# Optimization experiments

Measured on AMD Instinct MI355X. Metric: run time of the kernel, lower is better.

The kernel has to match this reference:

```python
import jax, jax.numpy as jnp
import numpy as np

EPS = 1e-5  # torch LayerNorm default

def _ln(x, g, b):
    m = jnp.mean(x, axis=-1, keepdims=True)
    v = jnp.var(x, axis=-1, keepdims=True)
    return (x - m) / jnp.sqrt(v + EPS) * g + b

def setup_inputs() -> dict:
    B, S, F, H = 32, 512, 32, 128
    key = jax.random.key(0)
    ks = jax.random.split(key, 20)
    sc = 0.05
    inp = {
        "x": jax.random.normal(ks[0], (B, S, F), dtype=jnp.float32),
        # per-feature GRNs, stacked along F. fc1: Linear(1,H) -> weight vec (F,H)
        "fw1": jax.random.normal(ks[1], (F, H), dtype=jnp.float32) * sc,
        "fb1": jax.random.normal(ks[2], (F, H), dtype=jnp.float32) * sc,
        "fw2": jax.random.normal(ks[3], (F, H, H), dtype=jnp.float32) * sc,
        "fb2": jax.random.normal(ks[4], (F, H), dtype=jnp.float32) * sc,
        "fglu_w": jax.random.normal(ks[5], (F, H, 2 * H), dtype=jnp.float32) * sc,
        "fglu_b": jax.random.normal(ks[6], (F, 2 * H), dtype=jnp.float32) * sc,
        "fskip": jax.random.normal(ks[7], (F, H), dtype=jnp.float32) * sc,  # skip_proj Linear(1,H,bias=False)
        "fln_g": jnp.ones((F, H), dtype=jnp.float32),
        "fln_b": jnp.zeros((F, H), dtype=jnp.float32),
        # weight GRN: Linear(F,H)->ELU->Linear(H,F)->GLU(F)->LN(F); skip is identity (F==F)
        "ww1": jax.random.normal(ks[8], (F, H), dtype=jnp.float32) * sc,
        "wb1": jax.random.normal(ks[9], (H,), dtype=jnp.float32) * sc,
        "ww2": jax.random.normal(ks[10], (H, F), dtype=jnp.float32) * sc,
        "wb2": jax.random.normal(ks[11], (F,), dtype=jnp.float32) * sc,
        "wglu_w": jax.random.normal(ks[12], (F, 2 * F), dtype=jnp.float32) * sc,
        "wglu_b": jax.random.normal(ks[13], (2 * F,), dtype=jnp.float32) * sc,
        "wln_g": jnp.ones((F,), dtype=jnp.float32),
        "wln_b": jnp.zeros((F,), dtype=jnp.float32),
    }
    return inp

def reference(x, fw1, fb1, fw2, fb2, fglu_w, fglu_b, fskip, fln_g, fln_b,
              ww1, wb1, ww2, wb2, wglu_w, wglu_b, wln_g, wln_b):
    # ---- per-feature GRNs, batched over the F axis (dropout = eval, identity) ----
    # fc1(Linear(1,H)) + ELU : x[...,f] is a scalar per token
    h = jax.nn.elu(x[..., None] * fw1 + fb1)                 # (B,S,F,H)
    h = jnp.einsum('bsfh,fho->bsfo', h, fw2) + fb2           # fc2 (B,S,F,H)
    g = jnp.einsum('bsfh,fho->bsfo', h, fglu_w) + fglu_b     # GLU pre-act (B,S,F,2H)
    v, gate = jnp.split(g, 2, axis=-1)
    glu = v * jax.nn.sigmoid(gate)                           # (B,S,F,H)
    skip = x[..., None] * fskip                              # skip_proj (B,S,F,H)
    processed = _ln(glu + skip, fln_g[None, None], fln_b[None, None])  # (B,S,F,H)

    # ---- weight GRN over the full feature vector ----
    wh = jax.nn.elu(jnp.einsum('bsf,fh->bsh', x, ww1) + wb1)  # (B,S,H)
    wh = jnp.einsum('bsh,hf->bsf', wh, ww2) + wb2             # (B,S,F)
    wg = jnp.einsum('bsf,fg->bsg', wh, wglu_w) + wglu_b       # (B,S,2F)
    wv, wgate = jnp.split(wg, 2, axis=-1)
    wglu = wv * jax.nn.sigmoid(wgate)
    w = _ln(wglu + x, wln_g, wln_b)                           # skip is identity (F==F)
    weights = jax.nn.softmax(w, axis=-1)                      # (B,S,F)

    out = jnp.einsum('bsf,bsfh->bsh', weights, processed)     # weighted combine
    return (out, weights)
```

## Files before the change

kernel.cpp:

```cpp
#include <hip/hip_runtime.h>
#include <cstdint>
#include <cstddef>

#define NTOK 16384
#define FDIM 32
#define HDIM 128
#define TOKB 32

typedef __attribute__((ext_vector_type(8))) short short8;
typedef __attribute__((ext_vector_type(4))) float float4v;
typedef __attribute__((ext_vector_type(2))) float float2v;
typedef __attribute__((ext_vector_type(4))) unsigned int uint4v;

__device__ __forceinline__ float elu_f(float x)  { return x > 0.f ? x : __expf(x) - 1.f; }
__device__ __forceinline__ float sigm_f(float x) { return 1.f / (1.f + __expf(-x)); }

__device__ __forceinline__ unsigned int f2bf(float f) {
  unsigned int u = __float_as_uint(f);
  u += 0x7FFFu + ((u >> 16) & 1u);
  return u >> 16;
}
__device__ __forceinline__ unsigned int cvtpk(float lo, float hi) {
  unsigned int r;
  asm("v_cvt_pk_bf16_f32 %0, %1, %2" : "=v"(r) : "v"(lo), "v"(hi));
  return r;
}

__global__ __launch_bounds__(256) void k_pw(
    const float* __restrict__ x,
    const float* __restrict__ fw2, const float* __restrict__ fb2,
    const float* __restrict__ fglu_w, const float* __restrict__ fglu_b,
    const float* __restrict__ fskip, const float* __restrict__ flng,
    const float* __restrict__ flnb,
    const float* __restrict__ ww1, const float* __restrict__ wb1,
    const float* __restrict__ ww2, const float* __restrict__ wb2,
    const float* __restrict__ wglu_w, const float* __restrict__ wglu_b,
    const float* __restrict__ wln_g, const float* __restrict__ wln_b,
    unsigned short* __restrict__ bfrag, float* __restrict__ scal,
    float* __restrict__ wout)
{
  __shared__ __align__(16) float smem[4096];
  const int tid = threadIdx.x;

  if (blockIdx.x < 128) {
    const int f  = blockIdx.x >> 2;
    const int ks = blockIdx.x & 3;
    const float* src = fw2 + ((size_t)f * 128 + ks * 32) * 128;
    for (int i = 0; i < 4; ++i) {
      int vi = tid + i * 256;
      *(float4v*)&smem[vi * 4] = *(const float4v*)&src[vi * 4];
    }
    __syncthreads();

    const int o2 = tid;
    float acc[32];
#pragma unroll
    for (int kk = 0; kk < 32; ++kk) acc[kk] = 0.f;
    float bacc = 0.f;

    for (int o = 0; o < 128; o += 4) {
      float gv0 = fglu_w[((size_t)f * 128 + o + 0) * 256 + o2];
      float gv1 = fglu_w[((size_t)f * 128 + o + 1) * 256 + o2];
      float gv2 = fglu_w[((size_t)f * 128 + o + 2) * 256 + o2];
      float gv3 = fglu_w[((size_t)f * 128 + o + 3) * 256 + o2];
      bacc += fb2[f * 128 + o + 0] * gv0 + fb2[f * 128 + o + 1] * gv1
            + fb2[f * 128 + o + 2] * gv2 + fb2[f * 128 + o + 3] * gv3;
#pragma unroll
      for (int kk = 0; kk < 32; ++kk) {
        float4v a4 = *(const float4v*)&smem[kk * 128 + o];
        acc[kk] += a4[0] * gv0 + a4[1] * gv1 + a4[2] * gv2 + a4[3] * gv3;
      }
    }

    const int type = o2 >> 7;
    const int h    = o2 & 127;
    const int w2   = h >> 4;
    const int r    = h & 15;
    const size_t tbase = ((((size_t)f * 8 + w2) * 2 + type) * 4 + ks) * 512;
#pragma unroll
    for (int gg = 0; gg < 4; ++gg) {
      uint4v pk;
      pk[0] = f2bf(acc[gg * 8 + 0]) | (f2bf(acc[gg * 8 + 1]) << 16);
      pk[1] = f2bf(acc[gg * 8 + 2]) | (f2bf(acc[gg * 8 + 3]) << 16);
      pk[2] = f2bf(acc[gg * 8 + 4]) | (f2bf(acc[gg * 8 + 5]) << 16);
      pk[3] = f2bf(acc[gg * 8 + 6]) | (f2bf(acc[gg * 8 + 7]) << 16);
      *(uint4v*)(bfrag + tbase + (size_t)(r + gg * 16) * 8) = pk;
    }
    if (ks == 0) {
      scal[f * 640 + type * 128 + h] = bacc + fglu_b[f * 256 + o2];
      if (type == 0) {
        scal[f * 640 + 256 + h] = fskip[f * 128 + h];
        scal[f * 640 + 384 + h] = flng[f * 128 + h];
        scal[f * 640 + 512 + h] = flnb[f * 128 + h];
      }
    }

  } else {
    const int bid = blockIdx.x - 128;
    const int wv  = tid >> 6;
    const int l   = tid & 63;
    const int t   = bid * 4 + wv;
    float* S = smem + wv * 256;

    float xv = x[(size_t)t * 32 + (l & 31)];
    if (l < 32) S[l] = xv;
    float a0 = wb1[l], a1 = wb1[l + 64];
    __syncthreads();
    for (int f2 = 0; f2 < 32; ++f2) {
      float xf = S[f2];
      a0 = fmaf(xf, ww1[f2 * 128 + l], a0);
      a1 = fmaf(xf, ww1[f2 * 128 + l + 64], a1);
    }
    a0 = elu_f(a0); a1 = elu_f(a1);
    S[32 + l] = a0; S[32 + l + 64] = a1;
    __syncthreads();

    const int o    = l & 31;
    const int half = l >> 5;
    float b = 0.f;
    for (int hh = 0; hh < 64; ++hh)
      b = fmaf(S[32 + half * 64 + hh], ww2[(half * 64 + hh) * 32 + o], b);
    b += __shfl_xor(b, 32);
    b += wb2[o];
    S[160 + o] = b;
    __syncthreads();

    float g = wglu_b[l];
    for (int o2i = 0; o2i < 32; ++o2i)
      g = fmaf(S[160 + o2i], wglu_w[o2i * 64 + l], g);

    float gate = __shfl_xor(g, 32);
    float y = g * sigm_f(gate) + xv;
    float s = y;
    s += __shfl_xor(s, 1); s += __shfl_xor(s, 2); s += __shfl_xor(s, 4);
    s += __shfl_xor(s, 8); s += __shfl_xor(s, 16);
    float mean = s * (1.f / 32.f);
    float d = y - mean;
    float ss = d * d;
    ss += __shfl_xor(ss, 1); ss += __shfl_xor(ss, 2); ss += __shfl_xor(ss, 4);
    ss += __shfl_xor(ss, 8); ss += __shfl_xor(ss, 16);
    float rstd = rsqrtf(ss * (1.f / 32.f) + 1e-5f);
    const int cc = l & 31;
    float ln = d * rstd * wln_g[cc] + wln_b[cc];
    float mx = ln;
    mx = fmaxf(mx, __shfl_xor(mx, 1));  mx = fmaxf(mx, __shfl_xor(mx, 2));
    mx = fmaxf(mx, __shfl_xor(mx, 4));  mx = fmaxf(mx, __shfl_xor(mx, 8));
    mx = fmaxf(mx, __shfl_xor(mx, 16));
    float e = __expf(ln - mx);
    float se = e;
    se += __shfl_xor(se, 1); se += __shfl_xor(se, 2); se += __shfl_xor(se, 4);
    se += __shfl_xor(se, 8); se += __shfl_xor(se, 16);
    if (l < 32) wout[(size_t)t * 32 + l] = e / se;
  }
}

__global__ __launch_bounds__(512, 4) void k_main(
    const float* __restrict__ x,
    const float* __restrict__ fw1, const float* __restrict__ fb1,
    const unsigned short* __restrict__ bfrag, const float* __restrict__ scal,
    const float* __restrict__ wts, float* __restrict__ out)
{
  __shared__ __align__(16) unsigned short a_lds[2][TOKB * 128];
  __shared__ __align__(16) float x_lds[FDIM * TOKB];
  __shared__ __align__(16) float w_lds[FDIM * TOKB];
  __shared__ __align__(16) float sred[3][2][TOKB];

  const int tid = threadIdx.x;
  const int w   = tid >> 6;
  const int l   = tid & 63;
  const int tk  = l & 15;
  const int rg  = l >> 4;
  const int t0  = blockIdx.x * TOKB;
  const int h0  = w * 16 + rg * 4;
  const int st  = tid >> 4;
  const int sk  = (tid & 15) * 8;
  const int stg_byte = (st * 256 + sk * 2) ^ ((st & 7) << 4);

  {
    float2v xv = *(const float2v*)(x   + (size_t)t0 * FDIM + tid * 2);
    float2v wv = *(const float2v*)(wts + (size_t)t0 * FDIM + tid * 2);
#pragma unroll
    for (int e = 0; e < 2; ++e) {
      int flat = tid * 2 + e;
      int tt = flat >> 5, ff = flat & 31;
      x_lds[ff * TOKB + tt] = xv[e];
      w_lds[ff * TOKB + tt] = wv[e];
    }
    if (tid < 192) ((float*)sred)[tid] = 0.f;
  }

  float4v oa0 = (float4v){0.f, 0.f, 0.f, 0.f};
  float4v oa1 = (float4v){0.f, 0.f, 0.f, 0.f};
  float4v py0, py1, plg, plb;
  float pwt0 = 0.f, pwt1 = 0.f;

  __syncthreads();

  int cb = 0;
#pragma unroll 1
  for (int f = 0; f < FDIM; ++f) {
    short8 aV[4], aG[4];
    {
      const unsigned short* bb = bfrag + (((size_t)f * 8 + w) * 8) * 512 + (size_t)l * 8;
#pragma unroll
      for (int ks = 0; ks < 4; ++ks) {
        aV[ks] = *(const short8*)(bb + (size_t)ks * 512);
        aG[ks] = *(const short8*)(bb + (size_t)(4 + ks) * 512);
      }
    }
    const float* sp = scal + (size_t)f * 640 + h0;
    float4v bcv = *(const float4v*)(sp);
    float4v bcg = *(const float4v*)(sp + 128);
    float4v fs4 = *(const float4v*)(sp + 256);
    float4v lg4 = *(const float4v*)(sp + 384);
    float4v lb4 = *(const float4v*)(sp + 512);
    float xt0 = x_lds[f * TOKB + tk],      wt0 = w_lds[f * TOKB + tk];
    float xt1 = x_lds[f * TOKB + 16 + tk], wt1 = w_lds[f * TOKB + 16 + tk];

    {
      float xf = x_lds[f * TOKB + st];
      float4v w1a = *(const float4v*)(fw1 + f * HDIM + sk);
      float4v w1b = *(const float4v*)(fw1 + f * HDIM + sk + 4);
      float4v b1a = *(const float4v*)(fb1 + f * HDIM + sk);
      float4v b1b = *(const float4v*)(fb1 + f * HDIM + sk + 4);
      uint4v pk;
      pk[0] = cvtpk(elu_f(fmaf(xf, w1a[0], b1a[0])),
                    elu_f(fmaf(xf, w1a[1], b1a[1])));
      pk[1] = cvtpk(elu_f(fmaf(xf, w1a[2], b1a[2])),
                    elu_f(fmaf(xf, w1a[3], b1a[3])));
      pk[2] = cvtpk(elu_f(fmaf(xf, w1b[0], b1b[0])),
                    elu_f(fmaf(xf, w1b[1], b1b[1])));
      pk[3] = cvtpk(elu_f(fmaf(xf, w1b[2], b1b[2])),
                    elu_f(fmaf(xf, w1b[3], b1b[3])));
      *(uint4v*)((char*)a_lds[f & 1] + stg_byte) = pk;
    }

    __syncthreads();

    float4v av0 = (float4v){0.f,0.f,0.f,0.f}, ag0 = av0, av1 = av0, ag1 = av0;
#pragma unroll
    for (int ks = 0; ks < 4; ++ks) {
      int b0 = tk * 256 + (ks * 32 + rg * 8) * 2;
      b0 ^= (tk & 7) << 4;
      short8 hf0 = *(const short8*)((const char*)a_lds[f & 1] + b0);
      int b1 = (16 + tk) * 256 + (ks * 32 + rg * 8) * 2;
      b1 ^= (tk & 7) << 4;
      short8 hf1 = *(const short8*)((const char*)a_lds[f & 1] + b1);
      av0 = __builtin_amdgcn_mfma_f32_16x16x32_bf16(aV[ks], hf0, av0, 0, 0, 0);
      ag0 = __builtin_amdgcn_mfma_f32_16x16x32_bf16(aG[ks], hf0, ag0, 0, 0, 0);
      av1 = __builtin_amdgcn_mfma_f32_16x16x32_bf16(aV[ks], hf1, av1, 0, 0, 0);
      ag1 = __builtin_amdgcn_mfma_f32_16x16x32_bf16(aG[ks], hf1, ag1, 0, 0, 0);
    }

    if (f > 0) {
      const int pb = (cb == 0) ? 2 : cb - 1;
      float sA  = sred[pb][0][tk],      ssA = sred[pb][1][tk];
      float sB  = sred[pb][0][16 + tk], ssB = sred[pb][1][16 + tk];
      float m0 = sA * (1.f / 128.f);
      float m1 = sB * (1.f / 128.f);
      float v0 = fmaf(-m0, m0, ssA * (1.f / 128.f));
      float v1 = fmaf(-m1, m1, ssB * (1.f / 128.f));
      float rw0 = rsqrtf(v0 + 1e-5f) * pwt0;
      float rw1 = rsqrtf(v1 + 1e-5f) * pwt1;
#pragma unroll
      for (int i = 0; i < 4; ++i) {
        oa0[i] = fmaf((py0[i] - m0) * rw0, plg[i], fmaf(pwt0, plb[i], oa0[i]));
        oa1[i] = fmaf((py1[i] - m1) * rw1, plg[i], fmaf(pwt1, plb[i], oa1[i]));
      }
    }

    float s0 = 0.f, ss0 = 0.f, s1 = 0.f, ss1 = 0.f;
#pragma unroll
    for (int i = 0; i < 4; ++i) {
      float ya = fmaf(xt0, fs4[i], (av0[i] + bcv[i]) * sigm_f(ag0[i] + bcg[i]));
      float yb = fmaf(xt1, fs4[i], (av1[i] + bcv[i]) * sigm_f(ag1[i] + bcg[i]));
      py0[i] = ya; py1[i] = yb;
      s0 += ya; ss0 = fmaf(ya, ya, ss0);
      s1 += yb; ss1 = fmaf(yb, yb, ss1);
    }
    s0  += __shfl_xor(s0, 16);  s0  += __shfl_xor(s0, 32);
    ss0 += __shfl_xor(ss0, 16); ss0 += __shfl_xor(ss0, 32);
    s1  += __shfl_xor(s1, 16);  s1  += __shfl_xor(s1, 32);
    ss1 += __shfl_xor(ss1, 16); ss1 += __shfl_xor(ss1, 32);
    if (rg == 0) {
      atomicAdd(&sred[cb][0][tk], s0);
      atomicAdd(&sred[cb][0][16 + tk], s1);
    } else if (rg == 1) {
      atomicAdd(&sred[cb][1][tk], ss0);
      atomicAdd(&sred[cb][1][16 + tk], ss1);
    }
    {
      const int nb = (cb == 2) ? 0 : cb + 1;
      if (tid < 64) ((float*)(sred[nb]))[tid] = 0.f;
    }

    pwt0 = wt0; pwt1 = wt1; plg = lg4; plb = lb4;
    cb = (cb == 2) ? 0 : cb + 1;
  }

  __syncthreads();
  {
    const int pb = (cb == 0) ? 2 : cb - 1;
    float sA  = sred[pb][0][tk],      ssA = sred[pb][1][tk];
    float sB  = sred[pb][0][16 + tk], ssB = sred[pb][1][16 + tk];
    float m0 = sA * (1.f / 128.f);
    float m1 = sB * (1.f / 128.f);
    float v0 = fmaf(-m0, m0, ssA * (1.f / 128.f));
    float v1 = fmaf(-m1, m1, ssB * (1.f / 128.f));
    float rw0 = rsqrtf(v0 + 1e-5f) * pwt0;
    float rw1 = rsqrtf(v1 + 1e-5f) * pwt1;
#pragma unroll
    for (int i = 0; i < 4; ++i) {
      oa0[i] = fmaf((py0[i] - m0) * rw0, plg[i], fmaf(pwt0, plb[i], oa0[i]));
      oa1[i] = fmaf((py1[i] - m1) * rw1, plg[i], fmaf(pwt1, plb[i], oa1[i]));
    }
  }

  *(float4v*)(out + (size_t)(t0 + tk) * HDIM + h0)      = oa0;
  *(float4v*)(out + (size_t)(t0 + 16 + tk) * HDIM + h0) = oa1;
}

extern "C" void kernel_launch(void* const* d_in, const int* in_sizes, int n_in,
                              void* d_out, int out_size, void* d_ws, size_t ws_size,
                              hipStream_t stream) {
  const float* x      = (const float*)d_in[0];
  const float* fw1    = (const float*)d_in[1];
  const float* fb1    = (const float*)d_in[2];
  const float* fw2    = (const float*)d_in[3];
  const float* fb2    = (const float*)d_in[4];
  const float* fglu_w = (const float*)d_in[5];
  const float* fglu_b = (const float*)d_in[6];
  const float* fskip  = (const float*)d_in[7];
  const float* fln_g  = (const float*)d_in[8];
  const float* fln_b  = (const float*)d_in[9];
  const float* ww1    = (const float*)d_in[10];
  const float* wb1    = (const float*)d_in[11];
  const float* ww2    = (const float*)d_in[12];
  const float* wb2    = (const float*)d_in[13];
  const float* wglu_w = (const float*)d_in[14];
  const float* wglu_b = (const float*)d_in[15];
  const float* wln_g  = (const float*)d_in[16];
  const float* wln_b  = (const float*)d_in[17];

  float* outp = (float*)d_out;
  float* wout = outp + (size_t)NTOK * HDIM;

  unsigned short* bfrag = (unsigned short*)d_ws;
  float* scal = (float*)((char*)d_ws + (size_t)2 * 1024 * 1024);

  k_pw<<<dim3(128 + NTOK / 4), dim3(256), 0, stream>>>(
      x, fw2, fb2, fglu_w, fglu_b, fskip, fln_g, fln_b,
      ww1, wb1, ww2, wb2, wglu_w, wglu_b, wln_g, wln_b,
      bfrag, scal, wout);
  k_main<<<dim3(NTOK / TOKB), dim3(512), 0, stream>>>(
      x, fw1, fb1, bfrag, scal, wout, outp);
}
```

Baseline: 143.7 us.

## Process two features per loop iteration to halve block barriers

The main loop now handles two features per iteration. Both feature tiles are staged into four LDS buffers, with one __syncthreads per pair instead of one per feature. The LayerNorm reduction buffers and deferred-combine state are duplicated so each pair's statistics are applied one iteration later. This cuts barrier count and lengthens the independent work between barriers, at the cost of more registers and LDS, which may hurt occupancy under launch_bounds(512,4).

```diff
diff --git a/kernel.cpp b/kernel.cpp
--- a/kernel.cpp
+++ b/kernel.cpp
@@ -160,10 +160,10 @@
     const unsigned short* __restrict__ bfrag, const float* __restrict__ scal,
     const float* __restrict__ wts, float* __restrict__ out)
 {
-  __shared__ __align__(16) unsigned short a_lds[2][TOKB * 128];
+  __shared__ __align__(16) unsigned short a_lds[4][TOKB * 128];
   __shared__ __align__(16) float x_lds[FDIM * TOKB];
   __shared__ __align__(16) float w_lds[FDIM * TOKB];
-  __shared__ __align__(16) float sred[3][2][TOKB];
+  __shared__ __align__(16) float sred[3][2][2][TOKB];
 
   const int tid = threadIdx.x;
   const int w   = tid >> 6;
@@ -186,43 +186,39 @@
       x_lds[ff * TOKB + tt] = xv[e];
       w_lds[ff * TOKB + tt] = wv[e];
     }
-    if (tid < 192) ((float*)sred)[tid] = 0.f;
+    if (tid < 384) ((float*)sred)[tid] = 0.f;
   }
 
   float4v oa0 = (float4v){0.f, 0.f, 0.f, 0.f};
   float4v oa1 = (float4v){0.f, 0.f, 0.f, 0.f};
-  float4v py0, py1, plg, plb;
-  float pwt0 = 0.f, pwt1 = 0.f;
+  float4v pyA0 = oa0, pyA1 = oa0, pyB0 = oa0, pyB1 = oa0;
+  float4v plgA = oa0, plbA = oa0, plgB = oa0, plbB = oa0;
+  float pwtA0 = 0.f, pwtA1 = 0.f, pwtB0 = 0.f, pwtB1 = 0.f;
 
   __syncthreads();
 
-  int cb = 0;
+  int p = 0;
 #pragma unroll 1
-  for (int f = 0; f < FDIM; ++f) {
+  for (int k = 0; k < FDIM / 2; ++k) {
+    const int g    = 2 * k;
+    const int bufp = (k & 1) * 2;
+
     short8 aV[4], aG[4];
     {
-      const unsigned short* bb = bfrag + (((size_t)f * 8 + w) * 8) * 512 + (size_t)l * 8;
+      const unsigned short* bb = bfrag + (((size_t)g * 8 + w) * 8) * 512 + (size_t)l * 8;
 #pragma unroll
       for (int ks = 0; ks < 4; ++ks) {
         aV[ks] = *(const short8*)(bb + (size_t)ks * 512);
         aG[ks] = *(const short8*)(bb + (size_t)(4 + ks) * 512);
       }
     }
-    const float* sp = scal + (size_t)f * 640 + h0;
-    float4v bcv = *(const float4v*)(sp);
-    float4v bcg = *(const float4v*)(sp + 128);
-    float4v fs4 = *(const float4v*)(sp + 256);
-    float4v lg4 = *(const float4v*)(sp + 384);
-    float4v lb4 = *(const float4v*)(sp + 512);
-    float xt0 = x_lds[f * TOKB + tk],      wt0 = w_lds[f * TOKB + tk];
-    float xt1 = x_lds[f * TOKB + 16 + tk], wt1 = w_lds[f * TOKB + 16 + tk];
-
-    {
-      float xf = x_lds[f * TOKB + st];
-      float4v w1a = *(const float4v*)(fw1 + f * HDIM + sk);
-      float4v w1b = *(const float4v*)(fw1 + f * HDIM + sk + 4);
-      float4v b1a = *(const float4v*)(fb1 + f * HDIM + sk);
-      float4v b1b = *(const float4v*)(fb1 + f * HDIM + sk + 4);
+
+    {
+      float xf = x_lds[g * TOKB + st];
+      float4v w1a = *(const float4v*)(fw1 + g * HDIM + sk);
+      float4v w1b = *(const float4v*)(fw1 + g * HDIM + sk + 4);
+      float4v b1a = *(const float4v*)(fb1 + g * HDIM + sk);
+      float4v b1b = *(const float4v*)(fb1 + g * HDIM + sk + 4);
       uint4v pk;
       pk[0] = cvtpk(elu_f(fmaf(xf, w1a[0], b1a[0])),
                     elu_f(fmaf(xf, w1a[1], b1a[1])));
@@ -232,87 +228,206 @@
                     elu_f(fmaf(xf, w1b[1], b1b[1])));
       pk[3] = cvtpk(elu_f(fmaf(xf, w1b[2], b1b[2])),
                     elu_f(fmaf(xf, w1b[3], b1b[3])));
-      *(uint4v*)((char*)a_lds[f & 1] + stg_byte) = pk;
+      *(uint4v*)((char*)a_lds[bufp] + stg_byte) = pk;
+    }
+    {
+      float xf = x_lds[(g + 1) * TOKB + st];
+      float4v w1a = *(const float4v*)(fw1 + (g + 1) * HDIM + sk);
+      float4v w1b = *(const float4v*)(fw1 + (g + 1) * HDIM + sk + 4);
+      float4v b1a = *(const float4v*)(fb1 + (g + 1) * HDIM + sk);
+      float4v b1b = *(const float4v*)(fb1 + (g + 1) * HDIM + sk + 4);
+      uint4v pk;
+      pk[0] = cvtpk(elu_f(fmaf(xf, w1a[0], b1a[0])),
+                    elu_f(fmaf(xf, w1a[1], b1a[1])));
+      pk[1] = cvtpk(elu_f(fmaf(xf, w1a[2], b1a[2])),
+                    elu_f(fmaf(xf, w1a[3], b1a[3])));
+      pk[2] = cvtpk(elu_f(fmaf(xf, w1b[0], b1b[0])),
+                    elu_f(fmaf(xf, w1b[1], b1b[1])));
+      pk[3] = cvtpk(elu_f(fmaf(xf, w1b[2], b1b[2])),
+                    elu_f(fmaf(xf, w1b[3], b1b[3])));
+      *(uint4v*)((char*)a_lds[bufp + 1] + stg_byte) = pk;
     }
 
     __syncthreads();
 
-    float4v av0 = (float4v){0.f,0.f,0.f,0.f}, ag0 = av0, av1 = av0, ag1 = av0;
-#pragma unroll
-    for (int ks = 0; ks < 4; ++ks) {
-      int b0 = tk * 256 + (ks * 32 + rg * 8) * 2;
-      b0 ^= (tk & 7) << 4;
-      short8 hf0 = *(const short8*)((const char*)a_lds[f & 1] + b0);
-      int b1 = (16 + tk) * 256 + (ks * 32 + rg * 8) * 2;
-      b1 ^= (tk & 7) << 4;
-      short8 hf1 = *(const short8*)((const char*)a_lds[f & 1] + b1);
-      av0 = __builtin_amdgcn_mfma_f32_16x16x32_bf16(aV[ks], hf0, av0, 0, 0, 0);
-      ag0 = __builtin_amdgcn_mfma_f32_16x16x32_bf16(aG[ks], hf0, ag0, 0, 0, 0);
-      av1 = __builtin_amdgcn_mfma_f32_16x16x32_bf16(aV[ks], hf1, av1, 0, 0, 0);
-      ag1 = __builtin_amdgcn_mfma_f32_16x16x32_bf16(aG[ks], hf1, ag1, 0, 0, 0);
-    }
-
-    if (f > 0) {
-      const int pb = (cb == 0) ? 2 : cb - 1;
-      float sA  = sred[pb][0][tk],      ssA = sred[pb][1][tk];
-      float sB  = sred[pb][0][16 + tk], ssB = sred[pb][1][16 + tk];
+    if (k > 0) {
+      const int pp = (p == 0) ? 2 : p - 1;
+      {
+        float sA  = sred[pp][0][0][tk],      ssA = sred[pp][0][1][tk];
+        float sB  = sred[pp][0][0][16 + tk], ssB = sred[pp][0][1][16 + tk];
+        float m0 = sA * (1.f / 128.f);
+        float m1 = sB * (1.f / 128.f);
+        float v0 = fmaf(-m0, m0, ssA * (1.f / 128.f));
+        float v1 = fmaf(-m1, m1, ssB * (1.f / 128.f));
+        float rw0 = rsqrtf(v0 + 1e-5f) * pwtA0;
+        float rw1 = rsqrtf(v1 + 1e-5f) * pwtA1;
+#pragma unroll
+        for (int i = 0; i < 4; ++i) {
+          oa0[i] = fmaf((pyA0[i] - m0) * rw0, plgA[i], fmaf(pwtA0, plbA[i], oa0[i]));
+          oa1[i] = fmaf((pyA1[i] - m1) * rw1, plgA[i], fmaf(pwtA1, plbA[i], oa1[i]));
+        }
+      }
+      {
+        float sA  = sred[pp][1][0][tk],      ssA = sred[pp][1][1][tk];
+        float sB  = sred[pp][1][0][16 + tk], ssB = sred[pp][1][1][16 + tk];
+        float m0 = sA * (1.f / 128.f);
+        float m1 = sB * (1.f / 128.f);
+        float v0 = fmaf(-m0, m0, ssA * (1.f / 128.f));
+        float v1 = fmaf(-m1, m1, ssB * (1.f / 128.f));
+        float rw0 = rsqrtf(v0 + 1e-5f) * pwtB0;
+        float rw1 = rsqrtf(v1 + 1e-5f) * pwtB1;
+#pragma unroll
+        for (int i = 0; i < 4; ++i) {
+          oa0[i] = fmaf((pyB0[i] - m0) * rw0, plgB[i], fmaf(pwtB0, plbB[i], oa0[i]));
+          oa1[i] = fmaf((pyB1[i] - m1) * rw1, plgB[i], fmaf(pwtB1, plbB[i], oa1[i]));
+        }
+      }
+    }
+
+    {
+      const float* sp = scal + (size_t)g * 640 + h0;
+      float4v bcv = *(const float4v*)(sp);
+      float4v bcg = *(const float4v*)(sp + 128);
+      float4v fs4 = *(const float4v*)(sp + 256);
+      float4v lg4 = *(const float4v*)(sp + 384);
+      float4v lb4 = *(const float4v*)(sp + 512);
+
+      float4v av0 = (float4v){0.f,0.f,0.f,0.f}, ag0 = av0, av1 = av0, ag1 = av0;
+#pragma unroll
+      for (int ks = 0; ks < 4; ++ks) {
+        int b0 = tk * 256 + (ks * 32 + rg * 8) * 2;
+        b0 ^= (tk & 7) << 4;
+        short8 hf0 = *(const short8*)((const char*)a_lds[bufp] + b0);
+        int b1 = (16 + tk) * 256 + (ks * 32 + rg * 8) * 2;
+        b1 ^= (tk & 7) << 4;
+        short8 hf1 = *(const short8*)((const char*)a_lds[bufp] + b1);
+        av0 = __builtin_amdgcn_mfma_f32_16x16x32_bf16(aV[ks], hf0, av0, 0, 0, 0);
+        ag0 = __builtin_amdgcn_mfma_f32_16x16x32_bf16(aG[ks], hf0, ag0, 0, 0, 0);
+        av1 = __builtin_amdgcn_mfma_f32_16x16x32_bf16(aV[ks], hf1, av1, 0, 0, 0);
+        ag1 = __builtin_amdgcn_mfma_f32_16x16x32_bf16(aG[ks], hf1, ag1, 0, 0, 0);
+      }
+
+      float xt0 = x_lds[g * TOKB + tk],      wt0 = w_lds[g * TOKB + tk];
+      float xt1 = x_lds[g * TOKB + 16 + tk], wt1 = w_lds[g * TOKB + 16 + tk];
+      float s0 = 0.f, ss0 = 0.f, s1 = 0.f, ss1 = 0.f;
+#pragma unroll
+      for (int i = 0; i < 4; ++i) {
+        float ya = fmaf(xt0, fs4[i], (av0[i] + bcv[i]) * sigm_f(ag0[i] + bcg[i]));
+        float yb = fmaf(xt1, fs4[i], (av1[i] + bcv[i]) * sigm_f(ag1[i] + bcg[i]));
+        pyA0[i] = ya; pyA1[i] = yb;
+        s0 += ya; ss0 = fmaf(ya, ya, ss0);
+        s1 += yb; ss1 = fmaf(yb, yb, ss1);
+      }
+      s0  += __shfl_xor(s0, 16);  s0  += __shfl_xor(s0, 32);
+      ss0 += __shfl_xor(ss0, 16); ss0 += __shfl_xor(ss0, 32);
+      s1  += __shfl_xor(s1, 16);  s1  += __shfl_xor(s1, 32);
+      ss1 += __shfl_xor(ss1, 16); ss1 += __shfl_xor(ss1, 32);
+      if (rg == 0) {
+        atomicAdd(&sred[p][0][0][tk], s0);
+        atomicAdd(&sred[p][0][0][16 + tk], s1);
+      } else if (rg == 1) {
+        atomicAdd(&sred[p][0][1][tk], ss0);
+        atomicAdd(&sred[p][0][1][16 + tk], ss1);
+      }
+      plgA = lg4; plbA = lb4; pwtA0 = wt0; pwtA1 = wt1;
+    }
+
+    {
+      const unsigned short* bb = bfrag + (((size_t)(g + 1) * 8 + w) * 8) * 512 + (size_t)l * 8;
+#pragma unroll
+      for (int ks = 0; ks < 4; ++ks) {
+        aV[ks] = *(const short8*)(bb + (size_t)ks * 512);
+        aG[ks] = *(const short8*)(bb + (size_t)(4 + ks) * 512);
+      }
+    }
+
+    {
+      const float* sp = scal + (size_t)(g + 1) * 640 + h0;
+      float4v bcv = *(const float4v*)(sp);
+      float4v bcg = *(const float4v*)(sp + 128);
+      float4v fs4 = *(const float4v*)(sp + 256);
+      float4v lg4 = *(const float4v*)(sp + 384);
+      float4v lb4 = *(const float4v*)(sp + 512);
+
+      float4v av0 = (float4v){0.f,0.f,0.f,0.f}, ag0 = av0, av1 = av0, ag1 = av0;
+#pragma unroll
+      for (int ks = 0; ks < 4; ++ks) {
+        int b0 = tk * 256 + (ks * 32 + rg * 8) * 2;
+        b0 ^= (tk & 7) << 4;
+        short8 hf0 = *(const short8*)((const char*)a_lds[bufp + 1] + b0);
+        int b1 = (16 + tk) * 256 + (ks * 32 + rg * 8) * 2;
+        b1 ^= (tk & 7) << 4;
+        short8 hf1 = *(const short8*)((const char*)a_lds[bufp + 1] + b1);
+        av0 = __builtin_amdgcn_mfma_f32_16x16x32_bf16(aV[ks], hf0, av0, 0, 0, 0);
+        ag0 = __builtin_amdgcn_mfma_f32_16x16x32_bf16(aG[ks], hf0, ag0, 0, 0, 0);
+        av1 = __builtin_amdgcn_mfma_f32_16x16x32_bf16(aV[ks], hf1, av1, 0, 0, 0);
+        ag1 = __builtin_amdgcn_mfma_f32_16x16x32_bf16(aG[ks], hf1, ag1, 0, 0, 0);
+      }
+
+      float xt0 = x_lds[(g + 1) * TOKB + tk],      wt0 = w_lds[(g + 1) * TOKB + tk];
+      float xt1 = x_lds[(g + 1) * TOKB + 16 + tk], wt1 = w_lds[(g + 1) * TOKB + 16 + tk];
+      float s0 = 0.f, ss0 = 0.f, s1 = 0.f, ss1 = 0.f;
+#pragma unroll
+      for (int i = 0; i < 4; ++i) {
+        float ya = fmaf(xt0, fs4[i], (av0[i] + bcv[i]) * sigm_f(ag0[i] + bcg[i]));
+        float yb = fmaf(xt1, fs4[i], (av1[i] + bcv[i]) * sigm_f(ag1[i] + bcg[i]));
+        pyB0[i] = ya; pyB1[i] = yb;
+        s0 += ya; ss0 = fmaf(ya, ya, ss0);
+        s1 += yb; ss1 = fmaf(yb, yb, ss1);
+      }
+      s0  += __shfl_xor(s0, 16);  s0  += __shfl_xor(s0, 32);
+      ss0 += __shfl_xor(ss0, 16); ss0 += __shfl_xor(ss0, 32);
+      s1  += __shfl_xor(s1, 16);  s1  += __shfl_xor(s1, 32);
+      ss1 += __shfl_xor(ss1, 16); ss1 += __shfl_xor(ss1, 32);
+      if (rg == 0) {
+        atomicAdd(&sred[p][1][0][tk], s0);
+        atomicAdd(&sred[p][1][0][16 + tk], s1);
+      } else if (rg == 1) {
+        atomicAdd(&sred[p][1][1][tk], ss0);
+        atomicAdd(&sred[p][1][1][16 + tk], ss1);
+      }
+      plgB = lg4; plbB = lb4; pwtB0 = wt0; pwtB1 = wt1;
+    }
+
+    {
+      const int pn = (p == 2) ? 0 : p + 1;
+      if (tid < 128) ((float*)(sred[pn]))[tid] = 0.f;
+      p = pn;
+    }
+  }
+
+  __syncthreads();
+  {
+    const int pp = (p == 0) ? 2 : p - 1;
+    {
+      float sA  = sred[pp][0][0][tk],      ssA = sred[pp][0][1][tk];
+      float sB  = sred[pp][0][0][16 + tk], ssB = sred[pp][0][1][16 + tk];
       float m0 = sA * (1.f / 128.f);
       float m1 = sB * (1.f / 128.f);
       float v0 = fmaf(-m0, m0, ssA * (1.f / 128.f));
       float v1 = fmaf(-m1, m1, ssB * (1.f / 128.f));
-      float rw0 = rsqrtf(v0 + 1e-5f) * pwt0;
-      float rw1 = rsqrtf(v1 + 1e-5f) * pwt1;
+      float rw0 = rsqrtf(v0 + 1e-5f) * pwtA0;
+      float rw1 = rsqrtf(v1 + 1e-5f) * pwtA1;
 #pragma unroll
       for (int i = 0; i < 4; ++i) {
-        oa0[i] = fmaf((py0[i] - m0) * rw0, plg[i], fmaf(pwt0, plb[i], oa0[i]));
-        oa1[i] = fmaf((py1[i] - m1) * rw1, plg[i], fmaf(pwt1, plb[i], oa1[i]));
-      }
-    }
-
-    float s0 = 0.f, ss0 = 0.f, s1 = 0.f, ss1 = 0.f;
-#pragma unroll
-    for (int i = 0; i < 4; ++i) {
-      float ya = fmaf(xt0, fs4[i], (av0[i] + bcv[i]) * sigm_f(ag0[i] + bcg[i]));
-      float yb = fmaf(xt1, fs4[i], (av1[i] + bcv[i]) * sigm_f(ag1[i] + bcg[i]));
-      py0[i] = ya; py1[i] = yb;
-      s0 += ya; ss0 = fmaf(ya, ya, ss0);
-      s1 += yb; ss1 = fmaf(yb, yb, ss1);
-    }
-    s0  += __shfl_xor(s0, 16);  s0  += __shfl_xor(s0, 32);
-    ss0 += __shfl_xor(ss0, 16); ss0 += __shfl_xor(ss0, 32);
-    s1  += __shfl_xor(s1, 16);  s1  += __shfl_xor(s1, 32);
-    ss1 += __shfl_xor(ss1, 16); ss1 += __shfl_xor(ss1, 32);
-    if (rg == 0) {
-      atomicAdd(&sred[cb][0][tk], s0);
-      atomicAdd(&sred[cb][0][16 + tk], s1);
-    } else if (rg == 1) {
-      atomicAdd(&sred[cb][1][tk], ss0);
-      atomicAdd(&sred[cb][1][16 + tk], ss1);
-    }
-    {
-      const int nb = (cb == 2) ? 0 : cb + 1;
-      if (tid < 64) ((float*)(sred[nb]))[tid] = 0.f;
-    }
-
-    pwt0 = wt0; pwt1 = wt1; plg = lg4; plb = lb4;
-    cb = (cb == 2) ? 0 : cb + 1;
-  }
-
-  __syncthreads();
-  {
-    const int pb = (cb == 0) ? 2 : cb - 1;
-    float sA  = sred[pb][0][tk],      ssA = sred[pb][1][tk];
-    float sB  = sred[pb][0][16 + tk], ssB = sred[pb][1][16 + tk];
-    float m0 = sA * (1.f / 128.f);
-    float m1 = sB * (1.f / 128.f);
-    float v0 = fmaf(-m0, m0, ssA * (1.f / 128.f));
-    float v1 = fmaf(-m1, m1, ssB * (1.f / 128.f));
-    float rw0 = rsqrtf(v0 + 1e-5f) * pwt0;
-    float rw1 = rsqrtf(v1 + 1e-5f) * pwt1;
-#pragma unroll
-    for (int i = 0; i < 4; ++i) {
-      oa0[i] = fmaf((py0[i] - m0) * rw0, plg[i], fmaf(pwt0, plb[i], oa0[i]));
-      oa1[i] = fmaf((py1[i] - m1) * rw1, plg[i], fmaf(pwt1, plb[i], oa1[i]));
+        oa0[i] = fmaf((pyA0[i] - m0) * rw0, plgA[i], fmaf(pwtA0, plbA[i], oa0[i]));
+        oa1[i] = fmaf((pyA1[i] - m1) * rw1, plgA[i], fmaf(pwtA1, plbA[i], oa1[i]));
+      }
+    }
+    {
+      float sA  = sred[pp][1][0][tk],      ssA = sred[pp][1][1][tk];
+      float sB  = sred[pp][1][0][16 + tk], ssB = sred[pp][1][1][16 + tk];
+      float m0 = sA * (1.f / 128.f);
+      float m1 = sB * (1.f / 128.f);
+      float v0 = fmaf(-m0, m0, ssA * (1.f / 128.f));
+      float v1 = fmaf(-m1, m1, ssB * (1.f / 128.f));
+      float rw0 = rsqrtf(v0 + 1e-5f) * pwtB0;
+      float rw1 = rsqrtf(v1 + 1e-5f) * pwtB1;
+#pragma unroll
+      for (int i = 0; i < 4; ++i) {
+        oa0[i] = fmaf((pyB0[i] - m0) * rw0, plgB[i], fmaf(pwtB0, plbB[i], oa0[i]));
+        oa1[i] = fmaf((pyB1[i] - m1) * rw1, plgB[i], fmaf(pwtB1, plbB[i], oa1[i]));
+      }
     }
   }
 
```

Result: faster. 139.2 us (-3.1%).
